# Optimization experiments

Measured on AMD Instinct MI355X. Metric: run time of the kernel, lower is better.

Reference implementation:

```python
import jax, jax.numpy as jnp
import numpy as np

B, CIN, F, H, W = 4, 256, 128, 64, 64
EPS = 1e-5

def _conv1x1(x, Wm, b):
    # x: [B,C,H,W], Wm: [O,C] (1x1 conv kernel), b: [O]
    return jnp.einsum('bchw,oc->bohw', x, Wm) + b[None, :, None, None]

def setup_inputs() -> dict:
    key = jax.random.key(0)
    ks = jax.random.split(key, 11)
    s_in = 1.0 / np.sqrt(CIN)
    s_f = 1.0 / np.sqrt(F)
    return {
        'x':    jax.random.normal(ks[0], (B, CIN, H, W), jnp.float32),
        'Wg':   jax.random.normal(ks[1], (F, CIN), jnp.float32) * s_in,
        'bg':   jax.random.normal(ks[2], (F,), jnp.float32) * s_in,
        'Wt':   jax.random.normal(ks[3], (F, CIN), jnp.float32) * s_in,
        'bt':   jax.random.normal(ks[4], (F,), jnp.float32) * s_in,
        'Wp':   jax.random.normal(ks[5], (F, CIN), jnp.float32) * s_in,
        'bp':   jax.random.normal(ks[6], (F,), jnp.float32) * s_in,
        'Wz':   jax.random.normal(ks[7], (CIN, F), jnp.float32) * s_f,
        'bz':   jax.random.normal(ks[8], (CIN,), jnp.float32) * s_f,
        'ln_w': jax.random.normal(ks[9], (CIN, H, W), jnp.float32) * 0.1,
        'ln_b': jax.random.normal(ks[10], (CIN, H, W), jnp.float32) * 0.1,
    }

def reference(x, Wg, bg, Wt, bt, Wp, bp, Wz, bz, ln_w, ln_b):
    b, _, h, w = x.shape
    n = h * w
    # 1x1 conv projections
    g = _conv1x1(x, Wg, bg).reshape(b, F, n).transpose(0, 2, 1)      # [B,N,F]
    theta = _conv1x1(x, Wt, bt).reshape(b, F, n).transpose(0, 2, 1)  # [B,N,F]
    phi = _conv1x1(x, Wp, bp).reshape(b, F, n)                        # [B,F,N]
    # embedded-Gaussian affinity + softmax attention
    f = jnp.einsum('bnf,bfm->bnm', theta, phi)                        # [B,N,N]
    attn = jax.nn.softmax(f, axis=-1)
    y = jnp.einsum('bnm,bmf->bnf', attn, g)                           # [B,N,F]
    y = y.transpose(0, 2, 1).reshape(b, F, h, w)                      # [B,F,H,W]
    # output projection
    z = _conv1x1(y, Wz, bz)                                           # [B,CIN,H,W]
    # LayerNorm over (C,H,W) per sample, affine params shaped [C,H,W]
    mu = jnp.mean(z, axis=(1, 2, 3), keepdims=True)
    var = jnp.var(z, axis=(1, 2, 3), keepdims=True)
    z = (z - mu) * jax.lax.rsqrt(var + EPS)
    z = z * ln_w[None] + ln_b[None]
    return z + x
```

## Files before the change

kernel.cpp:

```cpp
#include <hip/hip_runtime.h>
#include <stdint.h>

#define CIN 256
#define FDIM 128
#define NSP 4096
#define EPS 1e-5f

typedef __attribute__((ext_vector_type(8))) short short8;
typedef __attribute__((ext_vector_type(4))) float f32x4;
typedef __attribute__((ext_vector_type(16))) float f32x16;

__device__ __forceinline__ short f2bf(float f) {
  union { float f; uint32_t u; } v; v.f = f;
  uint32_t r = v.u + 0x7fffu + ((v.u >> 16) & 1u);
  return (short)(r >> 16);
}
__device__ __forceinline__ float bf2f(short h) {
  union { uint32_t u; float f; } v; v.u = ((uint32_t)(uint16_t)h) << 16;
  return v.f;
}

__global__ void prep_weights(const float* __restrict__ Wg, const float* __restrict__ Wt,
                             const float* __restrict__ Wp, const float* __restrict__ Wz,
                             short* __restrict__ Wbf, short* __restrict__ Wzbf) {
  int idx = blockIdx.x * 256 + threadIdx.x;
  if (idx < 384 * 256) {
    int row = idx >> 8, col = idx & 255;
    float v;
    if (row < 128)       v = Wt[row * 256 + col];
    else if (row < 256)  v = Wp[(row - 128) * 256 + col];
    else                 v = Wg[(row - 256) * 256 + col];
    Wbf[idx] = f2bf(v);
  } else {
    int j = idx - 384 * 256;
    if (j < 256 * 128) Wzbf[j] = f2bf(Wz[j]);
  }
}

__global__ void prep_xT(const float* __restrict__ x, short* __restrict__ xT) {
  __shared__ float tile[32][33];
  int b = blockIdx.z, c0 = blockIdx.y * 32, n0 = blockIdx.x * 32;
  int r = threadIdx.x >> 5, c = threadIdx.x & 31;
  const float* xb = x + (size_t)b * CIN * NSP;
#pragma unroll
  for (int k = 0; k < 4; k++)
    tile[r + 8 * k][c] = xb[(size_t)(c0 + r + 8 * k) * NSP + n0 + c];
  __syncthreads();
  short* xTb = xT + (size_t)b * NSP * CIN;
#pragma unroll
  for (int k = 0; k < 4; k++)
    xTb[(size_t)(n0 + r + 8 * k) * CIN + c0 + c] = f2bf(tile[c][r + 8 * k]);
}

__global__ void __launch_bounds__(256)
proj_kernel(const short* __restrict__ xT, const short* __restrict__ Wbf,
            const float* __restrict__ bt, const float* __restrict__ bp,
            const float* __restrict__ bg,
            short* __restrict__ theta, short* __restrict__ Kb, short* __restrict__ gT) {
  __shared__ short lds[5120];
  int bx = blockIdx.x;
  int b = bx >> 7;
  int n0 = (bx & 127) << 5;
  int p = blockIdx.y;
  int t = threadIdx.x, w = t >> 6, lane = t & 63, l15 = lane & 15, quad = lane >> 4;

  const short* arow = xT + (size_t)(b * NSP + n0 + (w & 1) * 16 + l15) * CIN;
  short8 a[8];
#pragma unroll
  for (int s = 0; s < 8; s++) a[s] = *(const short8*)(arow + s * 32 + quad * 8);

  const short* Wsrc = Wbf + p * 128 * 256;
  f32x4 zero = {0.f, 0.f, 0.f, 0.f};
  f32x4 acc[4];
#pragma unroll
  for (int i = 0; i < 4; i++) acc[i] = zero;

#pragma unroll
  for (int s = 0; s < 8; s++) {
#pragma unroll
    for (int ft = 0; ft < 4; ft++) {
      int ftg = (w >> 1) * 4 + ft;
      short8 bfr = *(const short8*)(Wsrc + (ftg * 16 + l15) * 256 + s * 32 + quad * 8);
      acc[ft] = __builtin_amdgcn_mfma_f32_16x16x32_bf16(a[s], bfr, acc[ft], 0, 0, 0);
    }
  }

  const float* bias = (p == 0) ? bt : (p == 1) ? bp : bg;
  if (p < 2) {
#pragma unroll
    for (int ft = 0; ft < 4; ft++) {
      int ftg = (w >> 1) * 4 + ft;
      float bv = bias[ftg * 16 + l15];
#pragma unroll
      for (int rr = 0; rr < 4; rr++) {
        int n = (w & 1) * 16 + quad * 4 + rr;
        lds[n * 136 + ftg * 16 + l15] = f2bf(acc[ft][rr] + bv);
      }
    }
    __syncthreads();
    short* dst = ((p == 0) ? theta : Kb) + (size_t)(b * NSP + n0) * FDIM;
#pragma unroll
    for (int i = 0; i < 2; i++) {
      int flat = t + 256 * i;
      int row = flat >> 4, ch = flat & 15;
      *(short8*)(dst + (size_t)row * FDIM + ch * 8) = *(const short8*)(lds + row * 136 + ch * 8);
    }
  } else {
#pragma unroll
    for (int ft = 0; ft < 4; ft++) {
      int ftg = (w >> 1) * 4 + ft;
      float bv = bias[ftg * 16 + l15];
#pragma unroll
      for (int rr = 0; rr < 4; rr++) {
        int n = (w & 1) * 16 + quad * 4 + rr;
        lds[(ftg * 16 + l15) * 40 + n] = f2bf(acc[ft][rr] + bv);
      }
    }
    __syncthreads();
    short* dst = gT + (size_t)b * FDIM * NSP + n0;
#pragma unroll
    for (int i = 0; i < 2; i++) {
      int flat = t + 256 * i;
      int f = flat >> 2, c = flat & 3;
      *(short8*)(dst + (size_t)f * NSP + c * 8) = *(const short8*)(lds + f * 40 + c * 8);
    }
  }
}

__global__ void __launch_bounds__(256, 2)
flash_kernel(const short* __restrict__ thetab, const short* __restrict__ Kb,
             const short* __restrict__ gT, short* __restrict__ opart,
             float* __restrict__ lpart) {
  __shared__ __attribute__((aligned(16))) char smem[66048];
  short* KldsA = (short*)smem;
  short* KldsB = (short*)(smem + 8704);
  short* VtA   = (short*)(smem + 17408);
  short* VtB   = (short*)(smem + 27648);
  float* Om    = (float*)smem;
  float* lsm   = (float*)(smem + 65536);

  const int bx = blockIdx.x;
  const int b  = bx >> 7;
  const int r  = bx & 127;
  const int q0 = (r >> 2) << 7;
  const int kc = r & 3;
  const int t = threadIdx.x, w = t >> 6, lane = t & 63;
  const int l31 = lane & 31, h = lane >> 5;
  const int qw = q0 + (w & 1) * 64;

  const short* Qsrc = thetab + (size_t)b * NSP * FDIM;
  const short* Ksrc = Kb + (size_t)b * NSP * FDIM;
  const short* Vsrc = gT + (size_t)b * FDIM * NSP;

  short8 qf0[8], qf1[8];
#pragma unroll
  for (int s = 0; s < 8; s++) {
    qf0[s] = *(const short8*)(Qsrc + (size_t)(qw + l31) * FDIM + s * 16 + h * 8);
    qf1[s] = *(const short8*)(Qsrc + (size_t)(qw + 32 + l31) * FDIM + s * 16 + h * 8);
  }

  f32x16 O0[4], O1[4];
#pragma unroll
  for (int i = 0; i < 4; i++) {
#pragma unroll
    for (int j = 0; j < 16; j++) { O0[i][j] = 0.f; O1[i][j] = 0.f; }
  }
  float lsum0 = 0.f, lsum1 = 0.f;

  const int kA0 = kc << 10;
  for (int j0 = 0; j0 < 512; j0 += 32) {
    __syncthreads();
    int kA = kA0 + j0, kB = kA + 512;
#pragma unroll
    for (int rep = 0; rep < 2; rep++) {
      int flat = t + 256 * rep;
      int row = flat >> 4, c = flat & 15;
      *(short8*)(KldsA + row * 136 + c * 8) =
          *(const short8*)(Ksrc + (size_t)(kA + row) * FDIM + c * 8);
      *(short8*)(KldsB + row * 136 + c * 8) =
          *(const short8*)(Ksrc + (size_t)(kB + row) * FDIM + c * 8);
      int f = flat >> 2, c2 = flat & 3;
      *(short8*)(VtA + f * 40 + c2 * 8) =
          *(const short8*)(Vsrc + (size_t)f * NSP + kA + c2 * 8);
      *(short8*)(VtB + f * 40 + c2 * 8) =
          *(const short8*)(Vsrc + (size_t)f * NSP + kB + c2 * 8);
    }
    __syncthreads();
    const short* Kl = (w & 2) ? KldsB : KldsA;
    const short* Vl = (w & 2) ? VtB : VtA;

    f32x16 S0, S1;
#pragma unroll
    for (int j = 0; j < 16; j++) { S0[j] = 0.f; S1[j] = 0.f; }
#pragma unroll
    for (int s = 0; s < 8; s++) {
      short8 ak = *(const short8*)(Kl + l31 * 136 + s * 16 + h * 8);
      S0 = __builtin_amdgcn_mfma_f32_32x32x16_bf16(ak, qf0[s], S0, 0, 0, 0);
      S1 = __builtin_amdgcn_mfma_f32_32x32x16_bf16(ak, qf1[s], S1, 0, 0, 0);
    }

    short8 Af0[2], Af1[2];
#pragma unroll
    for (int qb = 0; qb < 2; qb++) {
      float p[16];
      float ls = 0.f;
#pragma unroll
      for (int i = 0; i < 16; i++) {
        p[i] = __expf(qb ? S1[i] : S0[i]);
        ls += p[i];
      }
      if (qb) lsum1 += ls; else lsum0 += ls;
#pragma unroll
      for (int tt = 0; tt < 2; tt++) {
        const int rb = tt * 8;
        short8 af;
#pragma unroll
        for (int rr = 0; rr < 4; rr++) {
          float qv = h ? p[rb + rr] : p[rb + 4 + rr];
          float wv = __shfl_xor(qv, 32, 64);
          float e0 = h ? wv : p[rb + rr];
          float e1 = h ? p[rb + 4 + rr] : wv;
          af[rr] = f2bf(e0);
          af[4 + rr] = f2bf(e1);
        }
        if (qb) Af1[tt] = af; else Af0[tt] = af;
      }
    }

#pragma unroll
    for (int ft = 0; ft < 4; ft++) {
#pragma unroll
      for (int tt = 0; tt < 2; tt++) {
        short8 bv = *(const short8*)(Vl + (ft * 32 + l31) * 40 + tt * 16 + h * 8);
        O0[ft] = __builtin_amdgcn_mfma_f32_32x32x16_bf16(Af0[tt], bv, O0[ft], 0, 0, 0);
        O1[ft] = __builtin_amdgcn_mfma_f32_32x32x16_bf16(Af1[tt], bv, O1[ft], 0, 0, 0);
      }
    }
  }

  lsum0 += __shfl_xor(lsum0, 32, 64);
  lsum1 += __shfl_xor(lsum1, 32, 64);

  __syncthreads();
  if (w >= 2) {
    float* dst = Om + (size_t)(w - 2) * 8192;
#pragma unroll
    for (int qb = 0; qb < 2; qb++) {
#pragma unroll
      for (int ft = 0; ft < 4; ft++) {
#pragma unroll
        for (int reg = 0; reg < 16; reg++) {
          int rowq = qb * 32 + (reg & 3) + 8 * (reg >> 2) + 4 * h;
          dst[rowq * 128 + ft * 32 + l31] = qb ? O1[ft][reg] : O0[ft][reg];
        }
      }
    }
    if (h == 0) {
      lsm[(w - 2) * 64 + l31] = lsum0;
      lsm[(w - 2) * 64 + 32 + l31] = lsum1;
    }
  }
  __syncthreads();
  if (w < 2) {
    const float* src = Om + (size_t)w * 8192;
    short* od = opart + ((size_t)(kc * 4 + b) * NSP + qw) * FDIM;
#pragma unroll
    for (int qb = 0; qb < 2; qb++) {
#pragma unroll
      for (int ft = 0; ft < 4; ft++) {
#pragma unroll
        for (int reg = 0; reg < 16; reg++) {
          int rowq = qb * 32 + (reg & 3) + 8 * (reg >> 2) + 4 * h;
          float v = (qb ? O1[ft][reg] : O0[ft][reg]) + src[rowq * 128 + ft * 32 + l31];
          od[(size_t)rowq * FDIM + ft * 32 + l31] = f2bf(v);
        }
      }
    }
    if (h == 0) {
      size_t lb = (size_t)(kc * 4 + b) * NSP + qw;
      lpart[lb + l31] = lsum0 + lsm[w * 64 + l31];
      lpart[lb + 32 + l31] = lsum1 + lsm[w * 64 + 32 + l31];
    }
  }
}

__global__ void __launch_bounds__(256)
zproj_kernel(const short* __restrict__ opart, const float* __restrict__ lpart,
             const short* __restrict__ Wzbf, const float* __restrict__ bz,
             short* __restrict__ zb, float* __restrict__ psums) {
  __shared__ short ldsT[128 * 40];
  __shared__ float wsum[4][2];
  int bx = blockIdx.x;
  int b = bx >> 7;
  int n0 = (bx & 127) << 5;
  int ch0 = blockIdx.y * 128;
  int t = threadIdx.x, w = t >> 6, lane = t & 63, l15 = lane & 15, quad = lane >> 4;

  int row = n0 + (w & 1) * 16 + l15;
  float L = 0.f;
#pragma unroll
  for (int kcc = 0; kcc < 4; kcc++) L += lpart[(size_t)(kcc * 4 + b) * NSP + row];
  float inv = 1.0f / L;

  short8 a[4];
#pragma unroll
  for (int s = 0; s < 4; s++) {
    float accv[8] = {0, 0, 0, 0, 0, 0, 0, 0};
#pragma unroll
    for (int kcc = 0; kcc < 4; kcc++) {
      short8 v = *(const short8*)(opart + ((size_t)(kcc * 4 + b) * NSP + row) * FDIM + s * 32 + quad * 8);
#pragma unroll
      for (int j = 0; j < 8; j++) accv[j] += bf2f(v[j]);
    }
    short8 av;
#pragma unroll
    for (int j = 0; j < 8; j++) av[j] = f2bf(accv[j] * inv);
    a[s] = av;
  }

  f32x4 zero = {0.f, 0.f, 0.f, 0.f};
  f32x4 acc[4];
#pragma unroll
  for (int i = 0; i < 4; i++) acc[i] = zero;
#pragma unroll
  for (int s = 0; s < 4; s++) {
#pragma unroll
    for (int ct = 0; ct < 4; ct++) {
      int co = ch0 + (w >> 1) * 64 + ct * 16 + l15;
      short8 bfr = *(const short8*)(Wzbf + (size_t)co * FDIM + s * 32 + quad * 8);
      acc[ct] = __builtin_amdgcn_mfma_f32_16x16x32_bf16(a[s], bfr, acc[ct], 0, 0, 0);
    }
  }

  float s1 = 0.0f, s2 = 0.0f;
#pragma unroll
  for (int ct = 0; ct < 4; ct++) {
    int cg = (w >> 1) * 64 + ct * 16 + l15;
    float bv = bz[ch0 + cg];
#pragma unroll
    for (int rr = 0; rr < 4; rr++) {
      float v = acc[ct][rr] + bv;
      s1 += v; s2 += v * v;
      ldsT[cg * 40 + (w & 1) * 16 + quad * 4 + rr] = f2bf(v);
    }
  }
#pragma unroll
  for (int off = 32; off >= 1; off >>= 1) {
    s1 += __shfl_xor(s1, off, 64);
    s2 += __shfl_xor(s2, off, 64);
  }
  if (lane == 0) { wsum[w][0] = s1; wsum[w][1] = s2; }
  __syncthreads();
  if (t == 0) {
    int bid = blockIdx.y * 512 + bx;
    psums[bid * 2] = wsum[0][0] + wsum[1][0] + wsum[2][0] + wsum[3][0];
    psums[bid * 2 + 1] = wsum[0][1] + wsum[1][1] + wsum[2][1] + wsum[3][1];
  }
  short* dst = zb + (size_t)b * CIN * NSP + (size_t)ch0 * NSP + n0;
#pragma unroll
  for (int i = 0; i < 2; i++) {
    int flat = t + 256 * i;
    int c = flat >> 2, ch = flat & 3;
    *(short8*)(dst + (size_t)c * NSP + ch * 8) = *(const short8*)(ldsT + c * 40 + ch * 8);
  }
}

__global__ void reduce_sums(const float* __restrict__ psums, float* __restrict__ sums) {
  __shared__ float red[8];
  int t = threadIdx.x;
  if (t < 8) red[t] = 0.f;
  __syncthreads();
  for (int i = t; i < 1024; i += 256) {
    int b = (i & 511) >> 7;
    atomicAdd(&red[b * 2], psums[i * 2]);
    atomicAdd(&red[b * 2 + 1], psums[i * 2 + 1]);
  }
  __syncthreads();
  if (t < 8) sums[t] = red[t];
}

__global__ void __launch_bounds__(256)
finalize_kernel(const short* __restrict__ zbuf, const float* __restrict__ x,
                const float* __restrict__ lnw, const float* __restrict__ lnb,
                const float* __restrict__ sums, float* __restrict__ out) {
  int gid = blockIdx.x * 256 + threadIdx.x;
  size_t e0 = (size_t)gid * 8;
  int b = (int)(e0 >> 20);
  size_t ib = e0 & ((size_t)(1u << 20) - 1);
  float mean = sums[b * 2] * (1.0f / 1048576.0f);
  float var = sums[b * 2 + 1] * (1.0f / 1048576.0f) - mean * mean;
  float rs = rsqrtf(var + EPS);
  short8 zv = *(const short8*)(zbuf + e0);
#pragma unroll
  for (int k = 0; k < 8; k++) {
    float z = bf2f(zv[k]);
    out[e0 + k] = (z - mean) * rs * lnw[ib + k] + lnb[ib + k] + x[e0 + k];
  }
}

extern "C" void kernel_launch(void* const* d_in, const int* in_sizes, int n_in,
                              void* d_out, int out_size, void* d_ws, size_t ws_size,
                              hipStream_t stream) {
  const float* x   = (const float*)d_in[0];
  const float* Wg  = (const float*)d_in[1];
  const float* bg  = (const float*)d_in[2];
  const float* Wt  = (const float*)d_in[3];
  const float* bt  = (const float*)d_in[4];
  const float* Wp  = (const float*)d_in[5];
  const float* bp  = (const float*)d_in[6];
  const float* Wz  = (const float*)d_in[7];
  const float* bz  = (const float*)d_in[8];
  const float* lnw = (const float*)d_in[9];
  const float* lnb = (const float*)d_in[10];
  float* out = (float*)d_out;

  char* ws = (char*)d_ws;
  short* Wbf    = (short*)(ws);
  short* Wzbf   = (short*)(ws + 196608);
  short* xT     = (short*)(ws + 262144);
  short* opart  = (short*)(ws + 262144);
  float* lpart  = (float*)(ws + 17039360);
  short* thetab = (short*)(ws + 17301504);
  short* Kb     = (short*)(ws + 21495808);
  short* gT     = (short*)(ws + 25690112);
  short* zb     = (short*)(ws + 17301504);
  float* sums   = (float*)(ws + 29884416);
  float* psums  = (float*)(ws + 29884448);

  prep_weights<<<512, 256, 0, stream>>>(Wg, Wt, Wp, Wz, Wbf, Wzbf);
  prep_xT<<<dim3(128, 8, 4), 256, 0, stream>>>(x, xT);
  proj_kernel<<<dim3(512, 3), 256, 0, stream>>>(xT, Wbf, bt, bp, bg, thetab, Kb, gT);
  flash_kernel<<<512, 256, 0, stream>>>(thetab, Kb, gT, opart, lpart);
  zproj_kernel<<<dim3(512, 2), 256, 0, stream>>>(opart, lpart, Wzbf, bz, zb, psums);
  reduce_sums<<<1, 256, 0, stream>>>(psums, sums);
  finalize_kernel<<<2048, 256, 0, stream>>>(zb, x, lnw, lnb, sums, out);
}
```

Baseline: 212.2 us.

## Restructure flash kernel: per-wave 32-query tiles, double-buffered K/V prefetch, vectorized output

The flash attention kernel now gives each wave its own 32 query rows across the whole key chunk, instead of splitting keys between wave pairs and reducing the partial outputs through shared memory. K/V tiles are software-pipelined: the next tile's global loads are issued into registers before the current tile's MFMAs and written to the alternate LDS buffer afterwards, which removes one barrier per iteration. s_setprio is raised around the MFMA blocks, and the output goes through an LDS transpose so it can be written with 16-byte vector stores. The cross-wave reduction and its 64KB shared buffer are gone, but each wave now loops twice as many iterations with fewer independent MFMA chains (one accumulator set instead of two).

```diff
diff --git a/kernel.cpp b/kernel.cpp
--- a/kernel.cpp
+++ b/kernel.cpp
@@ -131,13 +131,7 @@
 flash_kernel(const short* __restrict__ thetab, const short* __restrict__ Kb,
              const short* __restrict__ gT, short* __restrict__ opart,
              float* __restrict__ lpart) {
-  __shared__ __attribute__((aligned(16))) char smem[66048];
-  short* KldsA = (short*)smem;
-  short* KldsB = (short*)(smem + 8704);
-  short* VtA   = (short*)(smem + 17408);
-  short* VtB   = (short*)(smem + 27648);
-  float* Om    = (float*)smem;
-  float* lsm   = (float*)(smem + 65536);
+  __shared__ __attribute__((aligned(16))) char smem[37888];
 
   const int bx = blockIdx.x;
   const int b  = bx >> 7;
@@ -146,142 +140,135 @@
   const int kc = r & 3;
   const int t = threadIdx.x, w = t >> 6, lane = t & 63;
   const int l31 = lane & 31, h = lane >> 5;
-  const int qw = q0 + (w & 1) * 64;
+  const int qw = q0 + w * 32;
 
   const short* Qsrc = thetab + (size_t)b * NSP * FDIM;
   const short* Ksrc = Kb + (size_t)b * NSP * FDIM;
   const short* Vsrc = gT + (size_t)b * FDIM * NSP;
 
-  short8 qf0[8], qf1[8];
-#pragma unroll
-  for (int s = 0; s < 8; s++) {
-    qf0[s] = *(const short8*)(Qsrc + (size_t)(qw + l31) * FDIM + s * 16 + h * 8);
-    qf1[s] = *(const short8*)(Qsrc + (size_t)(qw + 32 + l31) * FDIM + s * 16 + h * 8);
-  }
-
-  f32x16 O0[4], O1[4];
-#pragma unroll
-  for (int i = 0; i < 4; i++) {
-#pragma unroll
-    for (int j = 0; j < 16; j++) { O0[i][j] = 0.f; O1[i][j] = 0.f; }
-  }
-  float lsum0 = 0.f, lsum1 = 0.f;
+  short8 qf[8];
+#pragma unroll
+  for (int s = 0; s < 8; s++)
+    qf[s] = *(const short8*)(Qsrc + (size_t)(qw + l31) * FDIM + s * 16 + h * 8);
+
+  f32x16 O[4];
+#pragma unroll
+  for (int i = 0; i < 4; i++)
+#pragma unroll
+    for (int j = 0; j < 16; j++) O[i][j] = 0.f;
+  float lsum = 0.f;
+
+  const int kr0 = t >> 4, kcc0 = t & 15;
+  const int kr1 = 16 + (t >> 4);
+  const int vf0 = t >> 2, vcc0 = t & 3;
+  const int vf1 = 64 + (t >> 2);
 
   const int kA0 = kc << 10;
-  for (int j0 = 0; j0 < 512; j0 += 32) {
+  short8 rK0, rK1, rV0, rV1;
+
+  {
+    rK0 = *(const short8*)(Ksrc + (size_t)(kA0 + kr0) * FDIM + kcc0 * 8);
+    rK1 = *(const short8*)(Ksrc + (size_t)(kA0 + kr1) * FDIM + kcc0 * 8);
+    rV0 = *(const short8*)(Vsrc + (size_t)vf0 * NSP + kA0 + vcc0 * 8);
+    rV1 = *(const short8*)(Vsrc + (size_t)vf1 * NSP + kA0 + vcc0 * 8);
+    short* Kd = (short*)(smem);
+    short* Vd = (short*)(smem + 8704);
+    *(short8*)(Kd + kr0 * 136 + kcc0 * 8) = rK0;
+    *(short8*)(Kd + kr1 * 136 + kcc0 * 8) = rK1;
+    *(short8*)(Vd + vf0 * 40 + vcc0 * 8) = rV0;
+    *(short8*)(Vd + vf1 * 40 + vcc0 * 8) = rV1;
+  }
+
+#pragma unroll 2
+  for (int it = 0; it < 32; ++it) {
     __syncthreads();
-    int kA = kA0 + j0, kB = kA + 512;
-#pragma unroll
-    for (int rep = 0; rep < 2; rep++) {
-      int flat = t + 256 * rep;
-      int row = flat >> 4, c = flat & 15;
-      *(short8*)(KldsA + row * 136 + c * 8) =
-          *(const short8*)(Ksrc + (size_t)(kA + row) * FDIM + c * 8);
-      *(short8*)(KldsB + row * 136 + c * 8) =
-          *(const short8*)(Ksrc + (size_t)(kB + row) * FDIM + c * 8);
-      int f = flat >> 2, c2 = flat & 3;
-      *(short8*)(VtA + f * 40 + c2 * 8) =
-          *(const short8*)(Vsrc + (size_t)f * NSP + kA + c2 * 8);
-      *(short8*)(VtB + f * 40 + c2 * 8) =
-          *(const short8*)(Vsrc + (size_t)f * NSP + kB + c2 * 8);
-    }
-    __syncthreads();
-    const short* Kl = (w & 2) ? KldsB : KldsA;
-    const short* Vl = (w & 2) ? VtB : VtA;
-
-    f32x16 S0, S1;
-#pragma unroll
-    for (int j = 0; j < 16; j++) { S0[j] = 0.f; S1[j] = 0.f; }
+    if (it < 31) {
+      int kk = kA0 + (it + 1) * 32;
+      rK0 = *(const short8*)(Ksrc + (size_t)(kk + kr0) * FDIM + kcc0 * 8);
+      rK1 = *(const short8*)(Ksrc + (size_t)(kk + kr1) * FDIM + kcc0 * 8);
+      rV0 = *(const short8*)(Vsrc + (size_t)vf0 * NSP + kk + vcc0 * 8);
+      rV1 = *(const short8*)(Vsrc + (size_t)vf1 * NSP + kk + vcc0 * 8);
+    }
+    const short* Kl = (const short*)(smem + (it & 1) * 18944);
+    const short* Vl = (const short*)(smem + (it & 1) * 18944 + 8704);
+
+    f32x16 S;
+#pragma unroll
+    for (int j = 0; j < 16; j++) S[j] = 0.f;
+    __builtin_amdgcn_s_setprio(1);
 #pragma unroll
     for (int s = 0; s < 8; s++) {
       short8 ak = *(const short8*)(Kl + l31 * 136 + s * 16 + h * 8);
-      S0 = __builtin_amdgcn_mfma_f32_32x32x16_bf16(ak, qf0[s], S0, 0, 0, 0);
-      S1 = __builtin_amdgcn_mfma_f32_32x32x16_bf16(ak, qf1[s], S1, 0, 0, 0);
-    }
-
-    short8 Af0[2], Af1[2];
-#pragma unroll
-    for (int qb = 0; qb < 2; qb++) {
-      float p[16];
-      float ls = 0.f;
-#pragma unroll
-      for (int i = 0; i < 16; i++) {
-        p[i] = __expf(qb ? S1[i] : S0[i]);
-        ls += p[i];
+      S = __builtin_amdgcn_mfma_f32_32x32x16_bf16(ak, qf[s], S, 0, 0, 0);
+    }
+    __builtin_amdgcn_s_setprio(0);
+
+    float p[16];
+#pragma unroll
+    for (int i = 0; i < 16; i++) p[i] = __expf(S[i]);
+    float t8[8];
+#pragma unroll
+    for (int i = 0; i < 8; i++) t8[i] = p[2 * i] + p[2 * i + 1];
+    lsum += ((t8[0] + t8[1]) + (t8[2] + t8[3])) + ((t8[4] + t8[5]) + (t8[6] + t8[7]));
+
+    short8 Af[2];
+#pragma unroll
+    for (int tt = 0; tt < 2; tt++) {
+      const int rb = tt * 8;
+      short8 af;
+#pragma unroll
+      for (int rr = 0; rr < 4; rr++) {
+        float qv = h ? p[rb + rr] : p[rb + 4 + rr];
+        float wv = __shfl_xor(qv, 32, 64);
+        float e0 = h ? wv : p[rb + rr];
+        float e1 = h ? p[rb + 4 + rr] : wv;
+        af[rr] = f2bf(e0);
+        af[4 + rr] = f2bf(e1);
       }
-      if (qb) lsum1 += ls; else lsum0 += ls;
-#pragma unroll
-      for (int tt = 0; tt < 2; tt++) {
-        const int rb = tt * 8;
-        short8 af;
-#pragma unroll
-        for (int rr = 0; rr < 4; rr++) {
-          float qv = h ? p[rb + rr] : p[rb + 4 + rr];
-          float wv = __shfl_xor(qv, 32, 64);
-          float e0 = h ? wv : p[rb + rr];
-          float e1 = h ? p[rb + 4 + rr] : wv;
-          af[rr] = f2bf(e0);
-          af[4 + rr] = f2bf(e1);
-        }
-        if (qb) Af1[tt] = af; else Af0[tt] = af;
-      }
-    }
-
+      Af[tt] = af;
+    }
+
+    __builtin_amdgcn_s_setprio(1);
 #pragma unroll
     for (int ft = 0; ft < 4; ft++) {
 #pragma unroll
       for (int tt = 0; tt < 2; tt++) {
         short8 bv = *(const short8*)(Vl + (ft * 32 + l31) * 40 + tt * 16 + h * 8);
-        O0[ft] = __builtin_amdgcn_mfma_f32_32x32x16_bf16(Af0[tt], bv, O0[ft], 0, 0, 0);
-        O1[ft] = __builtin_amdgcn_mfma_f32_32x32x16_bf16(Af1[tt], bv, O1[ft], 0, 0, 0);
+        O[ft] = __builtin_amdgcn_mfma_f32_32x32x16_bf16(Af[tt], bv, O[ft], 0, 0, 0);
       }
     }
-  }
-
-  lsum0 += __shfl_xor(lsum0, 32, 64);
-  lsum1 += __shfl_xor(lsum1, 32, 64);
+    __builtin_amdgcn_s_setprio(0);
+
+    if (it < 31) {
+      short* Kd = (short*)(smem + ((it + 1) & 1) * 18944);
+      short* Vd = (short*)(smem + ((it + 1) & 1) * 18944 + 8704);
+      *(short8*)(Kd + kr0 * 136 + kcc0 * 8) = rK0;
+      *(short8*)(Kd + kr1 * 136 + kcc0 * 8) = rK1;
+      *(short8*)(Vd + vf0 * 40 + vcc0 * 8) = rV0;
+      *(short8*)(Vd + vf1 * 40 + vcc0 * 8) = rV1;
+    }
+  }
+
+  lsum += __shfl_xor(lsum, 32, 64);
 
   __syncthreads();
-  if (w >= 2) {
-    float* dst = Om + (size_t)(w - 2) * 8192;
-#pragma unroll
-    for (int qb = 0; qb < 2; qb++) {
-#pragma unroll
-      for (int ft = 0; ft < 4; ft++) {
-#pragma unroll
-        for (int reg = 0; reg < 16; reg++) {
-          int rowq = qb * 32 + (reg & 3) + 8 * (reg >> 2) + 4 * h;
-          dst[rowq * 128 + ft * 32 + l31] = qb ? O1[ft][reg] : O0[ft][reg];
-        }
-      }
-    }
-    if (h == 0) {
-      lsm[(w - 2) * 64 + l31] = lsum0;
-      lsm[(w - 2) * 64 + 32 + l31] = lsum1;
-    }
-  }
-  __syncthreads();
-  if (w < 2) {
-    const float* src = Om + (size_t)w * 8192;
-    short* od = opart + ((size_t)(kc * 4 + b) * NSP + qw) * FDIM;
-#pragma unroll
-    for (int qb = 0; qb < 2; qb++) {
-#pragma unroll
-      for (int ft = 0; ft < 4; ft++) {
-#pragma unroll
-        for (int reg = 0; reg < 16; reg++) {
-          int rowq = qb * 32 + (reg & 3) + 8 * (reg >> 2) + 4 * h;
-          float v = (qb ? O1[ft][reg] : O0[ft][reg]) + src[rowq * 128 + ft * 32 + l31];
-          od[(size_t)rowq * FDIM + ft * 32 + l31] = f2bf(v);
-        }
-      }
-    }
-    if (h == 0) {
-      size_t lb = (size_t)(kc * 4 + b) * NSP + qw;
-      lpart[lb + l31] = lsum0 + lsm[w * 64 + l31];
-      lpart[lb + 32 + l31] = lsum1 + lsm[w * 64 + 32 + l31];
-    }
-  }
+  short* tr = (short*)smem + w * 32 * 136;
+#pragma unroll
+  for (int ft = 0; ft < 4; ft++) {
+#pragma unroll
+    for (int reg = 0; reg < 16; reg++) {
+      int rowq = (reg & 3) + 8 * (reg >> 2) + 4 * h;
+      tr[rowq * 136 + ft * 32 + l31] = f2bf(O[ft][reg]);
+    }
+  }
+  short* od = opart + ((size_t)(kc * 4 + b) * NSP + qw) * FDIM;
+#pragma unroll
+  for (int i = 0; i < 8; i++) {
+    int slot = lane + 64 * i;
+    int row = slot >> 4, c = slot & 15;
+    *(short8*)(od + (size_t)row * FDIM + c * 8) = *(const short8*)(tr + row * 136 + c * 8);
+  }
+  if (h == 0) lpart[(size_t)(kc * 4 + b) * NSP + qw + l31] = lsum;
 }
 
 __global__ void __launch_bounds__(256)
```

Result: faster. 198.4 us (-6.5%).
